# Kernel optimization log

Measured on AMD Instinct MI355X. Metric: run time of the kernel, lower is better.

The kernel has to match this reference:

```python
import jax, jax.numpy as jnp
import numpy as np
from jax import lax

K = 3            # RFAConv kernel size
CIN = 66         # RFAConv in_channel = c2/2 + 2
UP = 64          # up channel count = c2/2
BN_EPS = 1e-5


def conv2d(x, w, stride=1, padding=0, groups=1, bias=None):
    out = lax.conv_general_dilated(
        x, w, (stride, stride), [(padding, padding), (padding, padding)],
        dimension_numbers=("NCHW", "OIHW", "NCHW"), feature_group_count=groups)
    if bias is not None:
        out = out + bias[None, :, None, None]
    return out


def avgpool3(x):
    # AvgPool2d(kernel=3, pad=1, stride=1), count_include_pad=True -> /9 everywhere
    s = lax.reduce_window(x, 0.0, lax.add, (1, 1, 3, 3), (1, 1, 1, 1),
                          [(0, 0), (0, 0), (1, 1), (1, 1)])
    return s / 9.0


def setup_inputs() -> dict:
    key = jax.random.key(0)
    ks = jax.random.split(key, 8)
    c1, c2 = 64, 128
    inp = {
        "x": jax.random.normal(ks[0], (8, c1, 256, 256), jnp.float32),
        "w_squeeze": jax.random.normal(ks[1], (c2, 4 * c1, 1, 1), jnp.float32) * 0.05,
        "w_gw": jax.random.normal(ks[2], (CIN * K * K, 1, 1, 1), jnp.float32) * 0.3,
        "w_gf": jax.random.normal(ks[3], (CIN * K * K, 1, K, K), jnp.float32) * 0.3,
        "bn_gamma": jnp.ones((CIN * K * K,), jnp.float32),
        "bn_beta": jnp.zeros((CIN * K * K,), jnp.float32),
        "bn_mean": jnp.zeros((CIN * K * K,), jnp.float32),
        "bn_var": jnp.ones((CIN * K * K,), jnp.float32),
        "w_conv": jax.random.normal(ks[4], (UP, CIN, K, K), jnp.float32) * 0.05,
        "b_conv": jnp.zeros((UP,), jnp.float32),
    }
    return inp


def reference(x, w_squeeze, w_gw, w_gf, bn_gamma, bn_beta, bn_mean, bn_var,
              w_conv, b_conv):
    # space_to_depth: [B,C,H,W] -> [B,4C,H/2,W/2]
    x = jnp.concatenate([x[..., ::2, ::2], x[..., 1::2, ::2],
                         x[..., ::2, 1::2], x[..., 1::2, 1::2]], axis=1)
    # squeeze0: 1x1 conv 4*c1 -> c2
    x = conv2d(x, w_squeeze)
    up, low = x[:, :UP], x[:, UP:]

    # AddCoords (with_r=False): append normalized xx (width) and yy (height)
    b, _, h, w = up.shape
    xx = (jnp.arange(w, dtype=up.dtype) / (w - 1) * 2.0 - 1.0)
    yy = (jnp.arange(h, dtype=up.dtype) / (h - 1) * 2.0 - 1.0)
    xx = jnp.broadcast_to(xx[None, None, None, :], (b, 1, h, w))
    yy = jnp.broadcast_to(yy[None, None, :, None], (b, 1, h, w))
    up = jnp.concatenate([up, xx, yy], axis=1)   # [b, 66, h, w]

    # RFAConv
    weight = conv2d(avgpool3(up), w_gw, groups=CIN)          # [b, 594, h, w]
    weight = jax.nn.softmax(weight.reshape(b, CIN, K * K, h, w), axis=2)

    feat = conv2d(up, w_gf, stride=1, padding=1, groups=CIN)  # [b, 594, h, w]
    scale = bn_gamma / jnp.sqrt(bn_var + BN_EPS)
    shift = bn_beta - bn_mean * scale
    feat = jax.nn.relu(feat * scale[None, :, None, None] + shift[None, :, None, None])
    feat = feat.reshape(b, CIN, K * K, h, w)

    wd = feat * weight
    # rearrange 'b c (n1 n2) h w -> b c (h n1) (w n2)'
    wd = wd.reshape(b, CIN, K, K, h, w).transpose(0, 1, 4, 2, 5, 3)
    wd = wd.reshape(b, CIN, h * K, w * K)
    up = conv2d(wd, w_conv, stride=K, bias=b_conv)            # [b, 64, h, w]

    y = jnp.concatenate([up, low], axis=1)                    # [b, 128, h, w]
    # channel shuffle: gather even channels then odd channels
    bb, n, hh, ww = y.shape
    y = y.reshape(bb, n // 2, 2, hh, ww)
    return jnp.concatenate([y[:, :, 0], y[:, :, 1]], axis=1)
```

## Files before the change

kernel.cpp:

```cpp
#include <hip/hip_runtime.h>
#include <math.h>

typedef __attribute__((ext_vector_type(8))) short short8;
typedef __attribute__((ext_vector_type(4))) float f32x4;

#define B 8
#define H 128
#define W 128
#define UPC 64
#define CIN 66
#define BN_EPS 1e-5f

#define UP_OFF   ((size_t)0)
#define BSQ_U16  ((size_t)16777216)
#define BSQ_CNT  32768
#define BF_U16   (BSQ_U16 + BSQ_CNT)
#define BF_CNT   38912
#define SC_F     ((size_t)8424448)
#define SH_F     (SC_F + 594)

static __device__ __forceinline__ unsigned short f2bf(float f) {
    unsigned u = __float_as_uint(f);
    u += 0x7fffu + ((u >> 16) & 1u);
    return (unsigned short)(u >> 16);
}
static __device__ __forceinline__ unsigned pack2(float lo, float hi) {
    return __builtin_amdgcn_perm(__float_as_uint(hi) + 0x8000u,
                                 __float_as_uint(lo) + 0x8000u, 0x07060302u);
}

__global__ void prep_kernel(const float* __restrict__ w_squeeze,
                            const float* __restrict__ gamma,
                            const float* __restrict__ beta,
                            const float* __restrict__ mean,
                            const float* __restrict__ var,
                            const float* __restrict__ w_conv,
                            float* __restrict__ ws)
{
    unsigned short* wsu = (unsigned short*)ws;
    int tid = blockIdx.x * blockDim.x + threadIdx.x;
    int nth = gridDim.x * blockDim.x;

    for (int idx = tid; idx < BSQ_CNT; idx += nth) {
        int j = idx & 7, lane = (idx >> 3) & 63, r = idx >> 9;
        int nt = r & 7, kc = r >> 3;
        int k = kc * 32 + ((lane >> 4) << 3) + j;
        int n = nt * 16 + (lane & 15);
        wsu[BSQ_U16 + idx] = f2bf(w_squeeze[n * 256 + k]);
    }
    for (int idx = tid; idx < BF_CNT; idx += nth) {
        int j = idx & 7, lane = (idx >> 3) & 63, r = idx >> 9;
        int nt = r & 3, ks = r >> 2;
        int k = ks * 32 + ((lane >> 4) << 3) + j;
        int n = nt * 16 + (lane & 15);
        float v = (k < 594) ? w_conv[n * 594 + k] : 0.f;
        wsu[BF_U16 + idx] = f2bf(v);
    }
    for (int i = tid; i < CIN * 9; i += nth) {
        float sc = gamma[i] / sqrtf(var[i] + BN_EPS);
        ws[SC_F + i] = sc;
        ws[SH_F + i] = beta[i] - mean[i] * sc;
    }
}

__global__ __launch_bounds__(256, 3) void squeeze_mfma(
    const float* __restrict__ x,
    float* __restrict__ wsp,
    float* __restrict__ out)
{
    __shared__ uint4 As[32 * 66];

    const int m0 = blockIdx.x * 64;
    const int w0 = m0 & 127;
    const int h  = (m0 >> 7) & 127;
    const int b  = m0 >> 14;
    const int tid  = threadIdx.x;
    const int lane = tid & 63;
    const int wv   = tid >> 6;

    const unsigned short* bsq = (const unsigned short*)wsp + BSQ_U16;
    short8 breg[2][8];
#pragma unroll
    for (int ks = 0; ks < 8; ++ks)
#pragma unroll
        for (int j = 0; j < 2; ++j)
            breg[j][ks] = *(const short8*)(bsq +
                (size_t)((ks * 8 + (2 * wv + j)) * 64 + lane) * 8);

#pragma unroll 2
    for (int it = 0; it < 4; ++it) {
        const int t = wv * 4 + it;
        const int gy = t & 1, oct = t >> 1;
        const size_t base = ((size_t)(b * 64 + oct * 8) * 256 + (2 * h + gy)) * 256
                          + 2 * (w0 + lane);
        float2 v[8];
#pragma unroll
        for (int i = 0; i < 8; ++i)
            v[i] = *(const float2*)(x + base + (size_t)i * 65536);
        uint4 lo, hi;
        lo.x = pack2(v[0].x, v[1].x); lo.y = pack2(v[2].x, v[3].x);
        lo.z = pack2(v[4].x, v[5].x); lo.w = pack2(v[6].x, v[7].x);
        hi.x = pack2(v[0].y, v[1].y); hi.y = pack2(v[2].y, v[3].y);
        hi.z = pack2(v[4].y, v[5].y); hi.w = pack2(v[6].y, v[7].y);
        As[(gy * 8 + oct) * 66 + lane]       = lo;
        As[((gy + 2) * 8 + oct) * 66 + lane] = hi;
    }
    __syncthreads();

    const int q = lane >> 4, m = lane & 15;
    f32x4 acc[4][2];
#pragma unroll
    for (int mt = 0; mt < 4; ++mt)
#pragma unroll
        for (int j = 0; j < 2; ++j) acc[mt][j] = (f32x4){0.f, 0.f, 0.f, 0.f};

#pragma unroll
    for (int ks = 0; ks < 8; ++ks)
#pragma unroll
        for (int mt = 0; mt < 4; ++mt) {
            short8 a = *(const short8*)&As[(ks * 4 + q) * 66 + mt * 16 + m];
            acc[mt][0] = __builtin_amdgcn_mfma_f32_16x16x32_bf16(a, breg[0][ks], acc[mt][0], 0, 0, 0);
            acc[mt][1] = __builtin_amdgcn_mfma_f32_16x16x32_bf16(a, breg[1][ks], acc[mt][1], 0, 0, 0);
        }

#pragma unroll
    for (int j = 0; j < 2; ++j) {
        const int oc = (2 * wv + j) * 16 + m;
#pragma unroll
        for (int mt = 0; mt < 4; ++mt)
#pragma unroll
            for (int r = 0; r < 4; ++r) {
                const int wc = w0 + mt * 16 + q * 4 + r;
                const float vv = acc[mt][j][r];
                if (oc < UPC) {
                    wsp[UP_OFF + ((size_t)((b * 64 + oc) * 128 + h)) * 128 + wc] = vv;
                } else {
                    const int lc = oc - 64;
                    const int ch = (lc & 1) ? (96 + ((lc - 1) >> 1)) : (32 + (lc >> 1));
                    out[((size_t)((b * 128 + ch) * 128 + h)) * 128 + wc] = vv;
                }
            }
    }
}

__device__ __forceinline__ void fs_from_n(
    int cu, const float n[9],
    const float* __restrict__ w_gw, const float* __restrict__ w_gf,
    const float* __restrict__ scp, const float* __restrict__ shp,
    float fs[9])
{
    const float p = (n[0] + n[1] + n[2] + n[3] + n[4] + n[5] + n[6] + n[7] + n[8]) * (1.f / 9.f);
    const float* gw = w_gw + cu * 9;
    const float* gf = w_gf + cu * 81;
    const float* sc = scp + cu * 9;
    const float* sh = shp + cu * 9;
    float e[9], se = 0.f;
#pragma unroll
    for (int j = 0; j < 9; ++j) { e[j] = __expf(p * gw[j]); se += e[j]; }
    const float sinv = 1.f / se;
#pragma unroll
    for (int j = 0; j < 9; ++j) {
        float cv = n[0] * gf[j * 9 + 0];
        cv = fmaf(n[1], gf[j * 9 + 1], cv); cv = fmaf(n[2], gf[j * 9 + 2], cv);
        cv = fmaf(n[3], gf[j * 9 + 3], cv); cv = fmaf(n[4], gf[j * 9 + 4], cv);
        cv = fmaf(n[5], gf[j * 9 + 5], cv); cv = fmaf(n[6], gf[j * 9 + 6], cv);
        cv = fmaf(n[7], gf[j * 9 + 7], cv); cv = fmaf(n[8], gf[j * 9 + 8], cv);
        float f = fmaf(cv, sc[j], sh[j]);
        fs[j] = fmaxf(f, 0.f) * (e[j] * sinv);
    }
}

__device__ __forceinline__ void pack_into(unsigned* pk, int ci, const float fs[9], float& carry)
{
    const int off = 9 * ci;
    if ((ci & 1) == 0) {
#pragma unroll
        for (int t = 0; t < 4; ++t) pk[off / 2 + t] = pack2(fs[2 * t], fs[2 * t + 1]);
        carry = fs[8];
    } else {
        pk[(off - 1) / 2] = pack2(carry, fs[0]);
#pragma unroll
        for (int t = 0; t < 4; ++t) pk[(off + 1) / 2 + t] = pack2(fs[1 + 2 * t], fs[2 + 2 * t]);
    }
}

template<bool BORDER>
__device__ __forceinline__ void chunk_fs(
    int cs, int wv, int lane, int h0, int w0,
    const float* __restrict__ upg,
    const float* __restrict__ w_gw, const float* __restrict__ w_gf,
    const float* __restrict__ scp, const float* __restrict__ shp,
    unsigned pk[36])
{
    const int px = lane & 7, py = lane >> 3;
    const int gy0 = h0 + py - 1, gx0 = w0 + px - 1;
    float carry = 0.f;
#pragma unroll
    for (int ci = 0; ci < 8; ++ci) {
        const int cu = __builtin_amdgcn_readfirstlane(cs + 8 * wv + ci);
        const float* cb = upg + (size_t)cu * (H * W) + gy0 * W + gx0;
        float n[9];
        if (!BORDER) {
#pragma unroll
            for (int dy = 0; dy < 3; ++dy)
#pragma unroll
                for (int dx = 0; dx < 3; ++dx)
                    n[dy * 3 + dx] = cb[dy * W + dx];
        } else {
#pragma unroll
            for (int dy = 0; dy < 3; ++dy)
#pragma unroll
                for (int dx = 0; dx < 3; ++dx) {
                    const int gy = gy0 + dy, gx = gx0 + dx;
                    const bool ok = ((unsigned)gy < 128u) & ((unsigned)gx < 128u);
                    n[dy * 3 + dx] = ok ? cb[dy * W + dx] : 0.f;
                }
        }
        float fs[9];
        fs_from_n(cu, n, w_gw, w_gf, scp, shp, fs);
        pack_into(pk, ci, fs, carry);
    }
}

__device__ __forceinline__ void coord_n(int which, int h0, int w0, int lane, float n[9])
{
    const int px = lane & 7, py = lane >> 3;
#pragma unroll
    for (int dy = 0; dy < 3; ++dy)
#pragma unroll
        for (int dx = 0; dx < 3; ++dx) {
            const int gy = h0 + py - 1 + dy, gx = w0 + px - 1 + dx;
            const bool ok = ((unsigned)gy < 128u) & ((unsigned)gx < 128u);
            const float v = (which == 0) ? (gx * (2.f / 127.f) - 1.f)
                                         : (gy * (2.f / 127.f) - 1.f);
            n[dy * 3 + dx] = ok ? v : 0.f;
        }
}

template<int NSTEPS>
__device__ __forceinline__ void do_mfma(
    int base, const uint4* As, const unsigned short* __restrict__ bfw,
    int wv, int lane, f32x4 acc[2][2])
{
    const int q = lane >> 4, m = lane & 15;
    const int ntb = (wv >> 1) * 2;
    const int pt0 = (wv & 1) * 2;
#pragma unroll
    for (int ks = 0; ks < NSTEPS; ++ks) {
        short8 b0 = *(const short8*)(bfw + (size_t)(((base + ks) * 4 + ntb + 0) * 64 + lane) * 8);
        short8 b1 = *(const short8*)(bfw + (size_t)(((base + ks) * 4 + ntb + 1) * 64 + lane) * 8);
#pragma unroll
        for (int mt = 0; mt < 2; ++mt) {
            short8 a = *(const short8*)&As[(ks * 4 + q) * 64 + (pt0 + mt) * 16 + m];
            acc[mt][0] = __builtin_amdgcn_mfma_f32_16x16x32_bf16(a, b0, acc[mt][0], 0, 0, 0);
            acc[mt][1] = __builtin_amdgcn_mfma_f32_16x16x32_bf16(a, b1, acc[mt][1], 0, 0, 0);
        }
    }
}

__global__ __launch_bounds__(256, 4) void fused_mfma(
    const float* __restrict__ wsp,
    const float* __restrict__ w_gw,
    const float* __restrict__ w_gf,
    const float* __restrict__ b_conv,
    float* __restrict__ out)
{
    __shared__ uint4 As[40 * 64];

    const int bx = blockIdx.x;
    const int w0 = (bx & 15) * 8;
    const int h0 = ((bx >> 4) & 15) * 8;
    const int b  = bx >> 8;
    const int tid = threadIdx.x, lane = tid & 63, wv = tid >> 6;
    const bool interior = (h0 > 0) & (h0 < 120) & (w0 > 0) & (w0 < 120);

    const float* upg = wsp + UP_OFF + (size_t)b * UPC * H * W;
    const float* scp = wsp + SC_F;
    const float* shp = wsp + SH_F;
    const unsigned short* bfw = (const unsigned short*)wsp + BF_U16;

    f32x4 acc[2][2];
#pragma unroll
    for (int mt = 0; mt < 2; ++mt)
#pragma unroll
        for (int j = 0; j < 2; ++j) acc[mt][j] = (f32x4){0.f, 0.f, 0.f, 0.f};

    {
        unsigned pk[36];
        if (interior) chunk_fs<false>(0, wv, lane, h0, w0, upg, w_gw, w_gf, scp, shp, pk);
        else          chunk_fs<true >(0, wv, lane, h0, w0, upg, w_gw, w_gf, scp, shp, pk);
        __syncthreads();
#pragma unroll
        for (int kb = 0; kb < 9; ++kb)
            As[(9 * wv + kb) * 64 + lane] =
                (uint4){pk[4 * kb], pk[4 * kb + 1], pk[4 * kb + 2], pk[4 * kb + 3]};
        __syncthreads();
        do_mfma<9>(0, As, bfw, wv, lane, acc);
    }

    {
        unsigned pk[36];
        if (interior) chunk_fs<false>(32, wv, lane, h0, w0, upg, w_gw, w_gf, scp, shp, pk);
        else          chunk_fs<true >(32, wv, lane, h0, w0, upg, w_gw, w_gf, scp, shp, pk);

        float fsA[9], fsB[9];
        if (wv == 3) {
            float n2[9];
            coord_n(0, h0, w0, lane, n2);
            fs_from_n(64, n2, w_gw, w_gf, scp, shp, fsA);
            coord_n(1, h0, w0, lane, n2);
            fs_from_n(65, n2, w_gw, w_gf, scp, shp, fsB);
        }
        __syncthreads();
#pragma unroll
        for (int kb = 0; kb < 9; ++kb)
            As[(9 * wv + kb) * 64 + lane] =
                (uint4){pk[4 * kb], pk[4 * kb + 1], pk[4 * kb + 2], pk[4 * kb + 3]};
        if (wv == 3) {
            uint4 v;
            v.x = pack2(fsA[0], fsA[1]); v.y = pack2(fsA[2], fsA[3]);
            v.z = pack2(fsA[4], fsA[5]); v.w = pack2(fsA[6], fsA[7]);
            As[36 * 64 + lane] = v;
            v.x = pack2(fsA[8], fsB[0]); v.y = pack2(fsB[1], fsB[2]);
            v.z = pack2(fsB[3], fsB[4]); v.w = pack2(fsB[5], fsB[6]);
            As[37 * 64 + lane] = v;
            v.x = pack2(fsB[7], fsB[8]); v.y = 0u; v.z = 0u; v.w = 0u;
            As[38 * 64 + lane] = v;
            v.x = 0u; v.y = 0u; v.z = 0u; v.w = 0u;
            As[39 * 64 + lane] = v;
        }
        __syncthreads();
        do_mfma<10>(9, As, bfw, wv, lane, acc);
    }

    const int q = lane >> 4, m = lane & 15;
    const int ntb = (wv >> 1) * 2, pt0 = (wv & 1) * 2;
#pragma unroll
    for (int mt = 0; mt < 2; ++mt)
#pragma unroll
        for (int j = 0; j < 2; ++j) {
            const int oc = (ntb + j) * 16 + m;
            const float bias = b_conv[oc];
            const int ch = (oc & 1) ? (64 + (oc >> 1)) : (oc >> 1);
#pragma unroll
            for (int r = 0; r < 4; ++r) {
                const int pix = (pt0 + mt) * 16 + q * 4 + r;
                out[((size_t)((b * 128 + ch) * 128 + (h0 + (pix >> 3)))) * 128
                    + (w0 + (pix & 7))] = acc[mt][j][r] + bias;
            }
        }
}

extern "C" void kernel_launch(void* const* d_in, const int* in_sizes, int n_in,
                              void* d_out, int out_size, void* d_ws, size_t ws_size,
                              hipStream_t stream)
{
    const float* x         = (const float*)d_in[0];
    const float* w_squeeze = (const float*)d_in[1];
    const float* w_gw      = (const float*)d_in[2];
    const float* w_gf      = (const float*)d_in[3];
    const float* gamma     = (const float*)d_in[4];
    const float* beta      = (const float*)d_in[5];
    const float* mean      = (const float*)d_in[6];
    const float* var       = (const float*)d_in[7];
    const float* w_conv    = (const float*)d_in[8];
    const float* b_conv    = (const float*)d_in[9];
    float* out = (float*)d_out;
    float* ws  = (float*)d_ws;

    prep_kernel<<<160, 256, 0, stream>>>(w_squeeze, gamma, beta, mean, var, w_conv, ws);
    squeeze_mfma<<<(B * H * W) / 64, 256, 0, stream>>>(x, ws, out);
    fused_mfma<<<B * 16 * 16, 256, 0, stream>>>(ws, w_gw, w_gf, b_conv, out);
}
```

Before: 367.2 us.

## Store up-branch intermediate as bf16 and stage 3x3 halos through LDS tiles

The squeeze kernel now reads x with float4 loads and writes the 64 up channels as packed bf16 instead of fp32, with vectorized float4 stores for the low half. The fused kernel reads those bf16 values into a per-wave LDS halo tile, software-pipelined one channel ahead, in place of nine scattered global loads per channel. Launch bounds are swapped between the two kernels. This cuts intermediate traffic in half and removes redundant neighbour loads, but rounds the intermediate activation to bf16, adding precision loss.

```diff
diff --git a/kernel.cpp b/kernel.cpp
--- a/kernel.cpp
+++ b/kernel.cpp
@@ -11,7 +11,6 @@
 #define CIN 66
 #define BN_EPS 1e-5f
 
-#define UP_OFF   ((size_t)0)
 #define BSQ_U16  ((size_t)16777216)
 #define BSQ_CNT  32768
 #define BF_U16   (BSQ_U16 + BSQ_CNT)
@@ -63,12 +62,12 @@
     }
 }
 
-__global__ __launch_bounds__(256, 3) void squeeze_mfma(
+__global__ __launch_bounds__(256, 4) void squeeze_mfma(
     const float* __restrict__ x,
     float* __restrict__ wsp,
     float* __restrict__ out)
 {
-    __shared__ uint4 As[32 * 66];
+    __shared__ uint4 As[32 * 64];
 
     const int m0 = blockIdx.x * 64;
     const int w0 = m0 & 127;
@@ -77,6 +76,32 @@
     const int tid  = threadIdx.x;
     const int lane = tid & 63;
     const int wv   = tid >> 6;
+    const int oct = tid >> 5;
+    const int pp  = tid & 31;
+
+    float4 v[2][8];
+#pragma unroll
+    for (int gy = 0; gy < 2; ++gy)
+#pragma unroll
+        for (int i = 0; i < 8; ++i)
+            v[gy][i] = *(const float4*)(x +
+                (size_t)(b * 64 + oct * 8 + i) * 65536 +
+                (2 * h + gy) * 256 + 2 * w0 + 4 * pp);
+
+#pragma unroll
+    for (int gy = 0; gy < 2; ++gy)
+#pragma unroll
+        for (int gx = 0; gx < 2; ++gx)
+#pragma unroll
+            for (int p = 0; p < 2; ++p) {
+                const int comp = p * 2 + gx;
+                uint4 u;
+                u.x = pack2(((const float*)&v[gy][0])[comp], ((const float*)&v[gy][1])[comp]);
+                u.y = pack2(((const float*)&v[gy][2])[comp], ((const float*)&v[gy][3])[comp]);
+                u.z = pack2(((const float*)&v[gy][4])[comp], ((const float*)&v[gy][5])[comp]);
+                u.w = pack2(((const float*)&v[gy][6])[comp], ((const float*)&v[gy][7])[comp]);
+                As[((gy + 2 * gx) * 8 + oct) * 64 + 2 * pp + p] = u;
+            }
 
     const unsigned short* bsq = (const unsigned short*)wsp + BSQ_U16;
     short8 breg[2][8];
@@ -87,24 +112,6 @@
             breg[j][ks] = *(const short8*)(bsq +
                 (size_t)((ks * 8 + (2 * wv + j)) * 64 + lane) * 8);
 
-#pragma unroll 2
-    for (int it = 0; it < 4; ++it) {
-        const int t = wv * 4 + it;
-        const int gy = t & 1, oct = t >> 1;
-        const size_t base = ((size_t)(b * 64 + oct * 8) * 256 + (2 * h + gy)) * 256
-                          + 2 * (w0 + lane);
-        float2 v[8];
-#pragma unroll
-        for (int i = 0; i < 8; ++i)
-            v[i] = *(const float2*)(x + base + (size_t)i * 65536);
-        uint4 lo, hi;
-        lo.x = pack2(v[0].x, v[1].x); lo.y = pack2(v[2].x, v[3].x);
-        lo.z = pack2(v[4].x, v[5].x); lo.w = pack2(v[6].x, v[7].x);
-        hi.x = pack2(v[0].y, v[1].y); hi.y = pack2(v[2].y, v[3].y);
-        hi.z = pack2(v[4].y, v[5].y); hi.w = pack2(v[6].y, v[7].y);
-        As[(gy * 8 + oct) * 66 + lane]       = lo;
-        As[((gy + 2) * 8 + oct) * 66 + lane] = hi;
-    }
     __syncthreads();
 
     const int q = lane >> 4, m = lane & 15;
@@ -118,28 +125,38 @@
     for (int ks = 0; ks < 8; ++ks)
 #pragma unroll
         for (int mt = 0; mt < 4; ++mt) {
-            short8 a = *(const short8*)&As[(ks * 4 + q) * 66 + mt * 16 + m];
+            short8 a = *(const short8*)&As[(ks * 4 + q) * 64 + mt * 16 + m];
             acc[mt][0] = __builtin_amdgcn_mfma_f32_16x16x32_bf16(a, breg[0][ks], acc[mt][0], 0, 0, 0);
             acc[mt][1] = __builtin_amdgcn_mfma_f32_16x16x32_bf16(a, breg[1][ks], acc[mt][1], 0, 0, 0);
         }
 
-#pragma unroll
-    for (int j = 0; j < 2; ++j) {
-        const int oc = (2 * wv + j) * 16 + m;
-#pragma unroll
-        for (int mt = 0; mt < 4; ++mt)
-#pragma unroll
-            for (int r = 0; r < 4; ++r) {
-                const int wc = w0 + mt * 16 + q * 4 + r;
-                const float vv = acc[mt][j][r];
-                if (oc < UPC) {
-                    wsp[UP_OFF + ((size_t)((b * 64 + oc) * 128 + h)) * 128 + wc] = vv;
-                } else {
-                    const int lc = oc - 64;
-                    const int ch = (lc & 1) ? (96 + ((lc - 1) >> 1)) : (32 + (lc >> 1));
-                    out[((size_t)((b * 128 + ch) * 128 + h)) * 128 + wc] = vv;
-                }
+    if (wv < 2) {
+        unsigned short* upw = (unsigned short*)wsp;
+#pragma unroll
+        for (int j = 0; j < 2; ++j) {
+            const int oc = (2 * wv + j) * 16 + m;
+#pragma unroll
+            for (int mt = 0; mt < 4; ++mt) {
+                uint2 st;
+                st.x = pack2(acc[mt][j][0], acc[mt][j][1]);
+                st.y = pack2(acc[mt][j][2], acc[mt][j][3]);
+                *(uint2*)(upw + (size_t)(b * 64 + oc) * 16384 + h * 128
+                          + (w0 + mt * 16 + q * 4)) = st;
             }
+        }
+    } else {
+#pragma unroll
+        for (int j = 0; j < 2; ++j) {
+            const int oc = (2 * wv + j) * 16 + m;
+            const int lc = oc - 64;
+            const int ch = (lc & 1) ? (96 + ((lc - 1) >> 1)) : (32 + (lc >> 1));
+#pragma unroll
+            for (int mt = 0; mt < 4; ++mt) {
+                float4 st = {acc[mt][j][0], acc[mt][j][1], acc[mt][j][2], acc[mt][j][3]};
+                *(float4*)(out + ((size_t)(b * 128 + ch) * 128 + h) * 128
+                           + (w0 + mt * 16 + q * 4)) = st;
+            }
+        }
     }
 }
 
@@ -184,44 +201,6 @@
     }
 }
 
-template<bool BORDER>
-__device__ __forceinline__ void chunk_fs(
-    int cs, int wv, int lane, int h0, int w0,
-    const float* __restrict__ upg,
-    const float* __restrict__ w_gw, const float* __restrict__ w_gf,
-    const float* __restrict__ scp, const float* __restrict__ shp,
-    unsigned pk[36])
-{
-    const int px = lane & 7, py = lane >> 3;
-    const int gy0 = h0 + py - 1, gx0 = w0 + px - 1;
-    float carry = 0.f;
-#pragma unroll
-    for (int ci = 0; ci < 8; ++ci) {
-        const int cu = __builtin_amdgcn_readfirstlane(cs + 8 * wv + ci);
-        const float* cb = upg + (size_t)cu * (H * W) + gy0 * W + gx0;
-        float n[9];
-        if (!BORDER) {
-#pragma unroll
-            for (int dy = 0; dy < 3; ++dy)
-#pragma unroll
-                for (int dx = 0; dx < 3; ++dx)
-                    n[dy * 3 + dx] = cb[dy * W + dx];
-        } else {
-#pragma unroll
-            for (int dy = 0; dy < 3; ++dy)
-#pragma unroll
-                for (int dx = 0; dx < 3; ++dx) {
-                    const int gy = gy0 + dy, gx = gx0 + dx;
-                    const bool ok = ((unsigned)gy < 128u) & ((unsigned)gx < 128u);
-                    n[dy * 3 + dx] = ok ? cb[dy * W + dx] : 0.f;
-                }
-        }
-        float fs[9];
-        fs_from_n(cu, n, w_gw, w_gf, scp, shp, fs);
-        pack_into(pk, ci, fs, carry);
-    }
-}
-
 __device__ __forceinline__ void coord_n(int which, int h0, int w0, int lane, float n[9])
 {
     const int px = lane & 7, py = lane >> 3;
@@ -258,65 +237,94 @@
     }
 }
 
-__global__ __launch_bounds__(256, 4) void fused_mfma(
+__global__ __launch_bounds__(256, 3) void fused_mfma(
     const float* __restrict__ wsp,
     const float* __restrict__ w_gw,
     const float* __restrict__ w_gf,
     const float* __restrict__ b_conv,
     float* __restrict__ out)
 {
-    __shared__ uint4 As[40 * 64];
+    __shared__ uint4          As[40 * 64];
+    __shared__ unsigned short tiles[4][160];
 
     const int bx = blockIdx.x;
     const int w0 = (bx & 15) * 8;
     const int h0 = ((bx >> 4) & 15) * 8;
     const int b  = bx >> 8;
     const int tid = threadIdx.x, lane = tid & 63, wv = tid >> 6;
+    const int px = lane & 7, py = lane >> 3;
     const bool interior = (h0 > 0) & (h0 < 120) & (w0 > 0) & (w0 < 120);
 
-    const float* upg = wsp + UP_OFF + (size_t)b * UPC * H * W;
+    const unsigned short* upb = (const unsigned short*)wsp + (size_t)b * UPC * 16384;
     const float* scp = wsp + SC_F;
     const float* shp = wsp + SH_F;
     const unsigned short* bfw = (const unsigned short*)wsp + BF_U16;
 
+    const int lr = lane >> 2, seg = lane & 3;
+    const bool loader = lr < 10;
+    int gyr = h0 - 1 + lr; gyr = min(max(gyr, 0), 127);
+    int c0w = w0 - 4 + seg * 4; c0w = min(max(c0w, 0), 124);
+    const size_t gposo = (size_t)gyr * 128 + c0w;
+    unsigned short* tw = &tiles[wv][0];
+    const int tco = lr * 16 + seg * 4;
+
     f32x4 acc[2][2];
 #pragma unroll
     for (int mt = 0; mt < 2; ++mt)
 #pragma unroll
         for (int j = 0; j < 2; ++j) acc[mt][j] = (f32x4){0.f, 0.f, 0.f, 0.f};
 
-    {
+#pragma unroll 1
+    for (int chunk = 0; chunk < 2; ++chunk) {
+        const int cbase = chunk * 32 + 8 * wv;
         unsigned pk[36];
-        if (interior) chunk_fs<false>(0, wv, lane, h0, w0, upg, w_gw, w_gf, scp, shp, pk);
-        else          chunk_fs<true >(0, wv, lane, h0, w0, upg, w_gw, w_gf, scp, shp, pk);
-        __syncthreads();
-#pragma unroll
-        for (int kb = 0; kb < 9; ++kb)
-            As[(9 * wv + kb) * 64 + lane] =
-                (uint4){pk[4 * kb], pk[4 * kb + 1], pk[4 * kb + 2], pk[4 * kb + 3]};
-        __syncthreads();
-        do_mfma<9>(0, As, bfw, wv, lane, acc);
-    }
-
-    {
-        unsigned pk[36];
-        if (interior) chunk_fs<false>(32, wv, lane, h0, w0, upg, w_gw, w_gf, scp, shp, pk);
-        else          chunk_fs<true >(32, wv, lane, h0, w0, upg, w_gw, w_gf, scp, shp, pk);
+        float carry = 0.f;
+        uint2 ldc, ldn;
+        if (loader) ldc = *(const uint2*)(upb + (size_t)cbase * 16384 + gposo);
+
+#pragma unroll
+        for (int ci = 0; ci < 8; ++ci) {
+            if (loader) *(uint2*)(tw + tco) = ldc;
+            if (ci < 7 && loader)
+                ldn = *(const uint2*)(upb + (size_t)(cbase + ci + 1) * 16384 + gposo);
+
+            float n[9];
+#pragma unroll
+            for (int dy = 0; dy < 3; ++dy)
+#pragma unroll
+                for (int dx = 0; dx < 3; ++dx) {
+                    unsigned uv = tw[(py + dy) * 16 + 3 + px + dx];
+                    float f = __uint_as_float(uv << 16);
+                    if (!interior) {
+                        const int gy = h0 + py - 1 + dy, gx = w0 + px - 1 + dx;
+                        const bool ok = ((unsigned)gy < 128u) & ((unsigned)gx < 128u);
+                        f = ok ? f : 0.f;
+                    }
+                    n[dy * 3 + dx] = f;
+                }
+
+            const int cu = __builtin_amdgcn_readfirstlane(cbase + ci);
+            float fs[9];
+            fs_from_n(cu, n, w_gw, w_gf, scp, shp, fs);
+            pack_into(pk, ci, fs, carry);
+            ldc = ldn;
+        }
 
         float fsA[9], fsB[9];
-        if (wv == 3) {
+        if (chunk == 1 && wv == 3) {
             float n2[9];
             coord_n(0, h0, w0, lane, n2);
             fs_from_n(64, n2, w_gw, w_gf, scp, shp, fsA);
             coord_n(1, h0, w0, lane, n2);
             fs_from_n(65, n2, w_gw, w_gf, scp, shp, fsB);
         }
+
         __syncthreads();
 #pragma unroll
         for (int kb = 0; kb < 9; ++kb)
             As[(9 * wv + kb) * 64 + lane] =
                 (uint4){pk[4 * kb], pk[4 * kb + 1], pk[4 * kb + 2], pk[4 * kb + 3]};
-        if (wv == 3) {
+        if (chunk == 1 && wv == 3) {
             uint4 v;
             v.x = pack2(fsA[0], fsA[1]); v.y = pack2(fsA[2], fsA[3]);
             v.z = pack2(fsA[4], fsA[5]); v.w = pack2(fsA[6], fsA[7]);
@@ -330,7 +338,9 @@
             As[39 * 64 + lane] = v;
         }
         __syncthreads();
-        do_mfma<10>(9, As, bfw, wv, lane, acc);
+
+        if (chunk == 0) do_mfma<9>(0, As, bfw, wv, lane, acc);
+        else            do_mfma<10>(9, As, bfw, wv, lane, acc);
     }
 
     const int q = lane >> 4, m = lane & 15;
```

Measured after the change: 458.4 us. +24.8%, slower.
